# Kernel tuning notes

Measured on AMD Instinct MI355X. Metric: run time of the kernel, lower is better.

Reference implementation:

```python
import jax, jax.numpy as jnp
import numpy as np

B, L, FD = 16, 196, 2048      # batch, fmap locations (14x14), resnet101 feat dim
N, WD, HD, DD = 1000, 300, 512, 5  # n_class, word_dim, hid_dim, d_dim
E, TMAX, NIMG = 50000, 5, 1000     # n_edges, gru steps, imagenet classes


def setup_inputs():
    key = jax.random.key(0)
    ks = jax.random.split(key, 32)
    p = lambda k, s: (jax.random.normal(k, s, jnp.float32) * 0.02)
    z = lambda n: jnp.zeros((n,), jnp.float32)
    return {
        'feats': jax.random.normal(ks[0], (B, L, FD), jnp.float32),
        'embed': jax.random.normal(ks[1], (N, WD), jnp.float32),
        'edges': jax.random.randint(ks[2], (2, E), 0, N, jnp.int32),
        # attention key/query nets
        'W_key': p(ks[3], (FD, HD)), 'b_key': z(HD),
        'W_query': p(ks[4], (WD, HD)), 'b_query': z(HD),
        # F_in: feat_dim -> 512 -> d_dim (relu)
        'Wf1': p(ks[5], (FD, 512)), 'bf1': z(512),
        'Wf2': p(ks[6], (512, DD)), 'bf2': z(DD),
        # F_rel: 2*word_dim -> 256 -> 1 (relu)
        'Wr1': p(ks[7], (2 * WD, 256)), 'br1': z(256),
        'Wr2': p(ks[8], (256, 1)), 'br2': z(1),
        # F_out: d_dim -> 512 -> 1 (relu)
        'Wo1': p(ks[9], (DD, 512)), 'bo1': z(512),
        'Wo2': p(ks[10], (512, 1)), 'bo2': z(1),
        # GRUCell (torch layout: [3*d, d] stacked r,z,n)
        'W_ih': p(ks[11], (3 * DD, DD)), 'b_ih': z(3 * DD),
        'W_hh': p(ks[12], (3 * DD, DD)), 'b_hh': z(3 * DD),
        # imagenet classifier on pooled features
        'W_clf': p(ks[13], (FD, NIMG)), 'b_clf': z(NIMG),
    }


def _gru_cell(x, h, W_ih, W_hh, b_ih, b_hh):
    gi = x @ W_ih.T + b_ih            # [M, 3d]
    gh = h @ W_hh.T + b_hh
    i_r, i_z, i_n = jnp.split(gi, 3, axis=-1)
    h_r, h_z, h_n = jnp.split(gh, 3, axis=-1)
    r = jax.nn.sigmoid(i_r + h_r)
    zg = jax.nn.sigmoid(i_z + h_z)
    n = jnp.tanh(i_n + r * h_n)
    return (1.0 - zg) * n + zg * h


def reference(feats, embed, edges, W_key, b_key, W_query, b_query,
              Wf1, bf1, Wf2, bf2, Wr1, br1, Wr2, br2, Wo1, bo1, Wo2, bo2,
              W_ih, b_ih, W_hh, b_hh, W_clf, b_clf):
    # imagenet scores from globally pooled backbone features
    pooled = jnp.mean(feats, axis=1)                      # [B, FD]
    imgnet_scores = jax.nn.softmax(pooled @ W_clf + b_clf, axis=1)

    # label-conditional spatial attention
    keys = feats @ W_key + b_key                          # [B, L, HD]
    queries = embed @ W_query + b_query                   # [N, HD]
    scores = jnp.einsum('blh,nh->bnl', keys, queries)     # [B, N, L]
    attn = jax.nn.softmax(scores, axis=2)
    graph_input = jnp.einsum('bnl,blf->bnf', attn, feats) # [B, N, FD]
    graph_input = graph_input.reshape(-1, FD)             # [B*N, FD]

    # F_in MLP -> initial hidden state
    h0 = jax.nn.relu(graph_input @ Wf1 + bf1) @ Wf2 + bf2  # [B*N, DD]

    # edge weights from word-embedding pairs, scattered into dense [N, N]
    et = jnp.concatenate([embed[edges[0]], embed[edges[1]]], axis=1)  # [E, 2*WD]
    vals = jnp.tanh((jax.nn.relu(et @ Wr1 + br1) @ Wr2 + br2).reshape(-1))
    prop_mat = jnp.zeros((N, N), jnp.float32).at[edges[0], edges[1]].add(vals)

    # t_max message-passing + GRU steps (sequential recurrence)
    def step(hidden, _):
        msg = jnp.tanh(jnp.einsum('nm,bmd->bnd', prop_mat,
                                  hidden.reshape(B, N, DD))).reshape(-1, DD)
        return _gru_cell(msg, hidden, W_ih, W_hh, b_ih, b_hh), None
    hidden, _ = jax.lax.scan(step, h0, None, length=TMAX)

    logits = (jax.nn.relu(hidden @ Wo1 + bo1) @ Wo2 + bo2).reshape(B, N)
    return logits, attn, imgnet_scores
```

## Files before the change

kernel.cpp:

```cpp
#include <hip/hip_runtime.h>
#include <hip/hip_bf16.h>
#include <math.h>

#define B_   16
#define L_   196
#define FD_  2048
#define N_   1000
#define WD_  300
#define HD_  512
#define DD_  5
#define E_   50000
#define TMAX_ 5
#define NIMG_ 1000
#define WDP_ 320
#define LP_  224
#define EKP_ 640

typedef __attribute__((ext_vector_type(8))) short bf16x8;
typedef __attribute__((ext_vector_type(4))) float f32x4;

#define SMEM_MEGA1    49152
#define SMEM_MM_SPLIT 49152
#define SMEM_MM_NS    24576
#define SMEM_PREP     4352

#define SBAR()    asm volatile("s_barrier" ::: "memory")
#define WVM(N)    asm volatile("s_waitcnt vmcnt(" #N ")" ::: "memory")

__device__ __forceinline__ short bf_hi(float x) {
    unsigned u = __float_as_uint(x);
    unsigned r = u + 0x7fffu + ((u >> 16) & 1u);
    return (short)(r >> 16);
}
__device__ __forceinline__ float bf2f_(short s) {
    return __uint_as_float(((unsigned)(unsigned short)s) << 16);
}

__device__ __forceinline__ void gl16(const short* g, char* l) {
    __builtin_amdgcn_global_load_lds(
        (const __attribute__((address_space(1))) void*)g,
        (__attribute__((address_space(3))) void*)l, 16, 0, 0);
}

#define OUT_SPLIT 1
#define OUT_SC    2
#define OUT_F1T   3
#define OUT_H0    4

template<int OUTMODE, bool SPLIT>
__device__ __forceinline__ void mm_core(
    char* sm, int bx, int by, int zb,
    const short* __restrict__ Ah, const short* __restrict__ Al,
    const short* __restrict__ Bh, const short* __restrict__ Bl,
    const float* __restrict__ bias, void* __restrict__ C0, void* __restrict__ C1,
    void* __restrict__ C2, const float* __restrict__ W2,
    int M, int N, int K, int kbeg, int kend)
{
    const int PBUF = SPLIT ? 24576 : 12288;
    char* AsH = sm;
    char* AsL = sm + 8192;
    char* BsH = sm + (SPLIT ? 16384 : 8192);
    char* BsL = sm + 20480;
    int t = threadIdx.x;
    int lane = t & 63, w = t >> 6;
    int q = lane >> 4, r = lane & 15;
    int row0 = by * 128, col0 = bx * 64;

    int srow = t >> 2, cd = t & 3;
    int cg = cd ^ ((srow >> 1) & 3);
    int gA0 = row0 + srow;       if (gA0 >= M) gA0 = M - 1;
    int gA1 = row0 + 64 + srow;  if (gA1 >= M) gA1 = M - 1;
    int gB  = col0 + srow;       if (gB  >= N) gB  = N - 1;
    const short* pA0 = Ah + (long)gA0 * K + cg * 8 + kbeg;
    const short* pA1 = Ah + (long)gA1 * K + cg * 8 + kbeg;
    const short* pB  = Bh + (long)gB  * K + cg * 8 + kbeg;
    const short* pA0l = Ah; const short* pA1l = Ah; const short* pBl = Bh;
    if (SPLIT) {
        pA0l = Al + (long)gA0 * K + cg * 8 + kbeg;
        pA1l = Al + (long)gA1 * K + cg * 8 + kbeg;
        pBl  = Bl + (long)gB  * K + cg * 8 + kbeg;
    }
    char* dA0 = AsH + t * 16;
    char* dA1 = AsH + 4096 + t * 16;
    char* dB  = BsH + t * 16;
    char* dA0l = AsL + t * 16;
    char* dA1l = AsL + 4096 + t * 16;
    char* dBl  = BsL + t * 16;

    int x = (q ^ ((r >> 1) & 3)) * 16;
    int aoff0 = (w * 32 + r) * 64 + x;
    int aoff1 = aoff0 + 1024;
    int boff[4];
    #pragma unroll
    for (int ct = 0; ct < 4; ct++) boff[ct] = (ct * 16 + r) * 64 + x;

    f32x4 zero4 = {0.f, 0.f, 0.f, 0.f};
    f32x4 acc[2][4];
    #pragma unroll
    for (int i = 0; i < 2; i++)
        #pragma unroll
        for (int j = 0; j < 4; j++) acc[i][j] = zero4;

    auto stage = [&](int ks) {
        int off = (ks & 1) * PBUF;
        int ko = ks * 32;
        gl16(pA0 + ko, dA0 + off);
        gl16(pA1 + ko, dA1 + off);
        gl16(pB  + ko, dB  + off);
        if (SPLIT) {
            gl16(pA0l + ko, dA0l + off);
            gl16(pA1l + ko, dA1l + off);
            gl16(pBl  + ko, dBl  + off);
        }
    };

    int nk = (kend - kbeg) >> 5;
    stage(0);
    for (int ks = 0; ks < nk; ks++) {
        if (ks + 1 < nk) {
            stage(ks + 1);
            if (SPLIT) { WVM(6); } else { WVM(3); }
        } else {
            WVM(0);
        }
        SBAR();

        int cur = (ks & 1) * PBUF;
        bf16x8 ah0 = *(const bf16x8*)(AsH + cur + aoff0);
        bf16x8 ah1 = *(const bf16x8*)(AsH + cur + aoff1);
        bf16x8 al0, al1;
        if (SPLIT) {
            al0 = *(const bf16x8*)(AsL + cur + aoff0);
            al1 = *(const bf16x8*)(AsL + cur + aoff1);
        }
        #pragma unroll
        for (int ct = 0; ct < 4; ct++) {
            bf16x8 bh = *(const bf16x8*)(BsH + cur + boff[ct]);
            acc[0][ct] = __builtin_amdgcn_mfma_f32_16x16x32_bf16(ah0, bh, acc[0][ct], 0, 0, 0);
            acc[1][ct] = __builtin_amdgcn_mfma_f32_16x16x32_bf16(ah1, bh, acc[1][ct], 0, 0, 0);
            if (SPLIT) {
                acc[0][ct] = __builtin_amdgcn_mfma_f32_16x16x32_bf16(al0, bh, acc[0][ct], 0, 0, 0);
                acc[1][ct] = __builtin_amdgcn_mfma_f32_16x16x32_bf16(al1, bh, acc[1][ct], 0, 0, 0);
                bf16x8 bl = *(const bf16x8*)(BsL + cur + boff[ct]);
                acc[0][ct] = __builtin_amdgcn_mfma_f32_16x16x32_bf16(ah0, bl, acc[0][ct], 0, 0, 0);
                acc[1][ct] = __builtin_amdgcn_mfma_f32_16x16x32_bf16(ah1, bl, acc[1][ct], 0, 0, 0);
            }
        }
        if (ks + 1 < nk) SBAR();
    }

    if (OUTMODE == OUT_H0) {
        float s[2][4][DD_];
        #pragma unroll
        for (int i = 0; i < 2; i++)
            #pragma unroll
            for (int reg = 0; reg < 4; reg++)
                #pragma unroll
                for (int d = 0; d < DD_; d++) s[i][reg][d] = 0.f;
        #pragma unroll
        for (int i = 0; i < 2; i++) {
            #pragma unroll
            for (int ct = 0; ct < 4; ct++) {
                int n = col0 + ct * 16 + r;
                float w2v[DD_];
                #pragma unroll
                for (int d = 0; d < DD_; d++) w2v[d] = W2[n * DD_ + d];
                float b1 = bias[n];
                #pragma unroll
                for (int reg = 0; reg < 4; reg++) {
                    int m = row0 + w * 32 + i * 16 + q * 4 + reg;
                    if (m >= M) continue;
                    float val = fmaxf(acc[i][ct][reg] + b1, 0.f);
                    #pragma unroll
                    for (int d = 0; d < DD_; d++) s[i][reg][d] = fmaf(val, w2v[d], s[i][reg][d]);
                }
            }
        }
        #pragma unroll
        for (int i = 0; i < 2; i++)
            #pragma unroll
            for (int reg = 0; reg < 4; reg++)
                #pragma unroll
                for (int d = 0; d < DD_; d++) {
                    float v = s[i][reg][d];
                    v += __shfl_xor(v, 1);
                    v += __shfl_xor(v, 2);
                    v += __shfl_xor(v, 4);
                    v += __shfl_xor(v, 8);
                    if (r == 0) {
                        int m = row0 + w * 32 + i * 16 + q * 4 + reg;
                        if (m < M)
                            atomicAdd(&((float*)C0)[(long)m * (B_ * DD_) + zb * DD_ + d], v);
                    }
                }
        return;
    }

    #pragma unroll
    for (int i = 0; i < 2; i++) {
        #pragma unroll
        for (int ct = 0; ct < 4; ct++) {
            #pragma unroll
            for (int reg = 0; reg < 4; reg++) {
                int m = row0 + w * 32 + i * 16 + q * 4 + reg;
                int n = col0 + ct * 16 + r;
                if (m >= M || n >= N) continue;
                float v = acc[i][ct][reg];
                if (OUTMODE == OUT_SC) {
                    ((float*)C0)[(long)m * N + n] = v;
                } else if (OUTMODE == OUT_F1T) {
                    int b = m / 196, l = m - b * 196;
                    ((short*)C2)[((long)b * 512 + n) * LP_ + l] = bf_hi(v);
                } else {
                    float v2 = v + bias[n];
                    long idx = (long)m * N + n;
                    short hi = bf_hi(v2);
                    ((short*)C0)[idx] = hi;
                    ((short*)C1)[idx] = bf_hi(v2 - bf2f_(hi));
                }
            }
        }
    }
}

__device__ __forceinline__ void edge_core(
    char* sm, int be,
    const short* __restrict__ embedH, const int* __restrict__ edges,
    const short* __restrict__ Wr1T, const float* __restrict__ br1,
    const float* __restrict__ Wr2, const float* __restrict__ br2,
    float* __restrict__ prop)
{
    const int EPBUF = 20480;
    char* As = sm;
    char* Bs = sm + 4096;
    int* src = (int*)(sm + 40960);
    int* dst = (int*)(sm + 41216);
    float (*part)[5] = (float(*)[5])(sm + 41472);
    int t = threadIdx.x;
    int e0 = be * 64;
    if (t < 64) {
        int e = e0 + t;
        src[t] = (e < E_) ? edges[e] : 0;
        dst[t] = (e < E_) ? edges[E_ + e] : 0;
    }
    __syncthreads();
    int lane = t & 63, w = t >> 6, q = lane >> 4, r = lane & 15;
    f32x4 zero4 = {0.f, 0.f, 0.f, 0.f};
    f32x4 acc[4][4];
    #pragma unroll
    for (int i = 0; i < 4; i++)
        #pragma unroll
        for (int j = 0; j < 4; j++) acc[i][j] = zero4;

    int srow = t >> 2, cd = t & 3;
    int cg = cd ^ ((srow >> 1) & 3);
    const short* baseS = embedH + (long)src[srow] * WDP_ + cg * 8;
    const short* baseD = embedH + (long)dst[srow] * WDP_ + cg * 8;
    const short* pB = Wr1T + (long)srow * EKP_ + cg * 8;
    char* dA = As + t * 16;
    char* dB = Bs + t * 16;

    int x = (q ^ ((r >> 1) & 3)) * 16;
    int aoff[4], boff[4];
    #pragma unroll
    for (int i = 0; i < 4; i++) {
        aoff[i] = (i * 16 + r) * 64 + x;
        boff[i] = (w * 64 + i * 16 + r) * 64 + x;
    }

    auto estage = [&](int ks) {
        int off = (ks & 1) * EPBUF;
        const short* pa = (ks < 10) ? baseS + ks * 32 : baseD + (ks - 10) * 32;
        gl16(pa, dA + off);
        #pragma unroll
        for (int i = 0; i < 4; i++)
            gl16(pB + (long)i * 64 * EKP_ + ks * 32, dB + i * 4096 + off);
    };

    estage(0);
    for (int ks = 0; ks < 20; ks++) {
        if (ks + 1 < 20) {
            estage(ks + 1);
            WVM(5);
        } else {
            WVM(0);
        }
        SBAR();

        int cur = (ks & 1) * EPBUF;
        bf16x8 af[4], bfr[4];
        #pragma unroll
        for (int rt = 0; rt < 4; rt++) af[rt] = *(const bf16x8*)(As + cur + aoff[rt]);
        #pragma unroll
        for (int ct = 0; ct < 4; ct++) bfr[ct] = *(const bf16x8*)(Bs + cur + boff[ct]);
        #pragma unroll
        for (int rt = 0; rt < 4; rt++)
            #pragma unroll
            for (int ct = 0; ct < 4; ct++)
                acc[rt][ct] = __builtin_amdgcn_mfma_f32_16x16x32_bf16(af[rt], bfr[ct], acc[rt][ct], 0, 0, 0);
        if (ks + 1 < 20) SBAR();
    }
    float b1v[4], w2v[4];
    #pragma unroll
    for (int ct = 0; ct < 4; ct++) {
        int u = w * 64 + ct * 16 + r;
        b1v[ct] = br1[u];
        w2v[ct] = Wr2[u];
    }
    #pragma unroll
    for (int rt = 0; rt < 4; rt++) {
        #pragma unroll
        for (int reg = 0; reg < 4; reg++) {
            float s = 0.f;
            #pragma unroll
            for (int ct = 0; ct < 4; ct++)
                s = fmaf(fmaxf(acc[rt][ct][reg] + b1v[ct], 0.f), w2v[ct], s);
            s += __shfl_xor(s, 1);
            s += __shfl_xor(s, 2);
            s += __shfl_xor(s, 4);
            s += __shfl_xor(s, 8);
            if (r == 0) part[rt * 16 + q * 4 + reg][w] = s;
        }
    }
    __syncthreads();
    if (t < 64 && e0 + t < E_) {
        float s = part[t][0] + part[t][1] + part[t][2] + part[t][3];
        atomicAdd(&prop[(long)src[t] * N_ + dst[t]], tanhf(s + br2[0]));
    }
}

__device__ __forceinline__ void transconv_core(
    char* sm, int bx, int by,
    const float* __restrict__ in, short* __restrict__ outH, short* __restrict__ outL,
    int Kd, int N, int Ks)
{
    float (*tile)[33] = (float(*)[33])sm;
    int k0 = bx * 32, n0 = by * 32;
    int t = threadIdx.x;
    int tr = t >> 5, tc = t & 31;
    #pragma unroll
    for (int i = 0; i < 4; i++) {
        int k = k0 + tr + i * 8, n = n0 + tc;
        tile[tr + i * 8][tc] = (k < Kd && n < N) ? in[(long)k * N + n] : 0.f;
    }
    __syncthreads();
    #pragma unroll
    for (int i = 0; i < 4; i++) {
        int n = n0 + tr + i * 8, k = k0 + tc;
        if (n < N && k < Ks) {
            float x = tile[tc][tr + i * 8];
            short hi = bf_hi(x);
            outH[(long)n * Ks + k] = hi;
            if (outL) outL[(long)n * Ks + k] = bf_hi(x - bf2f_(hi));
        }
    }
}

__global__ __launch_bounds__(256) void prep(
    float* __restrict__ prop, float* __restrict__ Ht0, const float* __restrict__ bf2,
    const float* __restrict__ feats, float* __restrict__ pooled,
    short* __restrict__ featsH, short* __restrict__ featsL,
    const float* __restrict__ embed, short* __restrict__ embH, short* __restrict__ embL,
    const float* __restrict__ W_key, const float* __restrict__ Wf1,
    short* __restrict__ WkfH, short* __restrict__ WkfL,
    const float* __restrict__ W_query, short* __restrict__ WqTh, short* __restrict__ WqTl,
    const float* __restrict__ Wr1, short* __restrict__ Wr1T, short* __restrict__ F1T)
{
    __shared__ __align__(16) char sm[SMEM_PREP];
    int b = blockIdx.x, t = threadIdx.x;
    if (b < 977) {
        int i = (b * 256 + t) * 4;
        if (i < N_ * N_) { float4 z = {0.f, 0.f, 0.f, 0.f}; *(float4*)(prop + i) = z; }
    } else if (b < 1290) {
        int i = (b - 977) * 256 + t;
        if (i < N_ * B_ * DD_) Ht0[i] = bf2[i % DD_];
    } else if (b < 1418) {
        int idx = (b - 1290) * 256 + t;
        int bb = idx / FD_, f = idx % FD_;
        const float* p = feats + (long)bb * L_ * FD_ + f;
        float acc = 0.f;
        for (int l = 0; l < L_; l++) acc += p[(long)l * FD_];
        pooled[idx] = acc * (1.0f / L_);
    } else if (b < 4554) {
        long i = ((long)(b - 1418) * 256 + t) * 8;
        float4 v0 = *(const float4*)(feats + i);
        float4 v1 = *(const float4*)(feats + i + 4);
        float xs[8] = {v0.x, v0.y, v0.z, v0.w, v1.x, v1.y, v1.z, v1.w};
        short h[8], l8[8];
        #pragma unroll
        for (int j = 0; j < 8; j++) {
            h[j] = bf_hi(xs[j]);
            l8[j] = bf_hi(xs[j] - bf2f_(h[j]));
        }
        *(int4*)(featsH + i) = *(int4*)h;
        *(int4*)(featsL + i) = *(int4*)l8;
    } else if (b < 4867) {
        int i = ((b - 4554) * 256 + t) * 4;
        if (i < N_ * WDP_) {
            int n = i / WDP_, c = i - n * WDP_;
            short h[4], l4[4];
            if (c < WD_) {
                float4 v = *(const float4*)(embed + (long)n * WD_ + c);
                float xs[4] = {v.x, v.y, v.z, v.w};
                #pragma unroll
                for (int j = 0; j < 4; j++) {
                    h[j] = bf_hi(xs[j]);
                    l4[j] = bf_hi(xs[j] - bf2f_(h[j]));
                }
            } else {
                #pragma unroll
                for (int j = 0; j < 4; j++) { h[j] = 0; l4[j] = 0; }
            }
            *(int2*)(embH + (long)n * WDP_ + c) = *(int2*)h;
            *(int2*)(embL + (long)n * WDP_ + c) = *(int2*)l4;
        }
    } else if (b < 5891) {
        int bb = b - 4867;
        transconv_core(sm, bb % 64, bb / 64, W_key, WkfH, WkfL, FD_, HD_, FD_);
    } else if (b < 6915) {
        int bb = b - 5891;
        transconv_core(sm, bb % 64, bb / 64, Wf1, WkfH + (size_t)512 * FD_, nullptr, FD_, HD_, FD_);
    } else if (b < 7075) {
        int bb = b - 6915;
        transconv_core(sm, bb % 10, bb / 10, W_query, WqTh, WqTl, WD_, HD_, WDP_);
    } else if (b < 7235) {
        int bb = b - 7075;
        int bx = bb % 20, by = bb / 20;
        float (*tile)[33] = (float(*)[33])sm;
        int k0 = bx * 32, n0 = by * 32;
        int tr = t >> 5, tc = t & 31;
        #pragma unroll
        for (int i = 0; i < 4; i++) {
            int kout = k0 + tr + i * 8, n = n0 + tc;
            int kin = (kout < 320) ? kout : kout - 20;
            bool valid = (kout < 320) ? (kout < 300) : (kout < 620);
            tile[tr + i * 8][tc] = valid ? Wr1[(long)kin * 256 + n] : 0.f;
        }
        __syncthreads();
        #pragma unroll
        for (int i = 0; i < 4; i++) {
            int n = n0 + tr + i * 8, k = k0 + tc;
            Wr1T[(long)n * EKP_ + k] = bf_hi(tile[tc][tr + i * 8]);
        }
    } else {
        int idx = (b - 7235) * 256 + t;
        int row = idx / 7, j = idx - row * 7;
        int2 z2; z2.x = 0; z2.y = 0;
        *(int2*)(F1T + (long)row * LP_ + 196 + j * 4) = z2;
    }
}

__global__ __launch_bounds__(256) void mega1(
    const short* __restrict__ featsH, const short* __restrict__ featsL,
    const short* __restrict__ WkfH, const short* __restrict__ WkfL,
    const float* __restrict__ b_key, short* __restrict__ keysH, short* __restrict__ keysL,
    short* __restrict__ F1T,
    const short* __restrict__ embH, const short* __restrict__ embL,
    const short* __restrict__ WqTh, const short* __restrict__ WqTl,
    const float* __restrict__ b_query, short* __restrict__ qH, short* __restrict__ qL,
    const int* __restrict__ edges, const short* __restrict__ Wr1T,
    const float* __restrict__ br1, const float* __restrict__ Wr2,
    const float* __restrict__ br2, float* __restrict__ prop,
    const float* __restrict__ pooled, const float* __restrict__ W_clf,
    const float* __restrict__ b_clf, float* __restrict__ Pimg)
{
    __shared__ __align__(16) char sm[SMEM_MEGA1];
    int b = blockIdx.x;
    if (b < 200) {
        int l = (b & 7) * 25 + (b >> 3);
        mm_core<OUT_SPLIT, true>(sm, l & 7, l >> 3, 0,
            featsH, featsL, WkfH, WkfL, b_key,
            keysH, keysL, nullptr, nullptr, B_ * L_, 512, FD_, 0, FD_);
    } else if (b < 400) {
        int bb = b - 200;
        int l = (bb & 7) * 25 + (bb >> 3);
        mm_core<OUT_F1T, false>(sm, l & 7, l >> 3, 0,
            featsH, nullptr, WkfH + (size_t)512 * FD_, nullptr, nullptr,
            nullptr, nullptr, F1T, nullptr, B_ * L_, 512, FD_, 0, FD_);
    } else if (b < 464) {
        int bb = b - 400;
        int l = (bb & 7) * 8 + (bb >> 3);
        mm_core<OUT_SPLIT, true>(sm, l & 7, l >> 3, 0,
            embH, embL, WqTh, WqTl, b_query,
            qH, qL, nullptr, nullptr, N_, HD_, WDP_, 0, WDP_);
    } else if (b < 1246) {
        edge_core(sm, b - 464, embH, edges, Wr1T, br1, Wr2, br2, prop);
    } else {
        int bb = b - 1246;
        int ks = bb / 63, ix = bb % 63;
        int i = ix * 256 + threadIdx.x;
        if (i < B_ * NIMG_) {
            int bi = i / NIMG_, n = i % NIMG_;
            const float* p = pooled + (long)bi * FD_ + ks * 256;
            const float* w = W_clf + (long)(ks * 256) * NIMG_ + n;
            float acc = (ks == 0) ? b_clf[n] : 0.f;
            #pragma unroll 4
            for (int k = 0; k < 256; k++) acc = fmaf(p[k], w[(long)k * NIMG_], acc);
            Pimg[(long)ks * (B_ * NIMG_) + i] = acc;
        }
    }
}

__global__ __launch_bounds__(256) void mega2(
    const short* __restrict__ qH, const short* __restrict__ qL,
    const short* __restrict__ keysH, const short* __restrict__ keysL,
    float* __restrict__ Pattn,
    const float* __restrict__ Pimg, float* __restrict__ out_img)
{
    __shared__ __align__(16) char sm[SMEM_MM_SPLIT];
    int b = blockIdx.x;
    if (b < 512) {
        int l = (b & 7) * 64 + (b >> 3);
        int zb = l >> 5, by = (l >> 2) & 7, bx = l & 3;
        const short* Bh = keysH + (long)zb * L_ * HD_;
        const short* Bl = keysL + (long)zb * L_ * HD_;
        float* C0 = Pattn + (long)zb * N_ * L_;
        mm_core<OUT_SC, true>(sm, bx, by, 0, qH, qL, Bh, Bl, nullptr,
                              C0, nullptr, nullptr, nullptr,
                              N_, L_, HD_, 0, HD_);
    } else {
        int t = threadIdx.x;
        int wave = (b - 512) * 4 + (t >> 6), lane = t & 63;
        if (wave >= B_) return;
        const int PER = (NIMG_ + 63) / 64;
        float v[PER];
        float m = -1e30f;
        int cnt = 0;
        for (int k = lane; k < NIMG_; k += 64) {
            float s = 0.f;
            #pragma unroll
            for (int ks = 0; ks < 8; ks++) s += Pimg[(long)ks * (B_ * NIMG_) + wave * NIMG_ + k];
            v[cnt] = s; m = fmaxf(m, s); cnt++;
        }
        #pragma unroll
        for (int off = 32; off; off >>= 1) m = fmaxf(m, __shfl_xor(m, off));
        float s = 0.f;
        for (int i = 0; i < cnt; i++) { v[i] = expf(v[i] - m); s += v[i]; }
        #pragma unroll
        for (int off = 32; off; off >>= 1) s += __shfl_xor(s, off);
        float inv = 1.f / s;
        cnt = 0;
        for (int k = lane; k < NIMG_; k += 64) out_img[(long)wave * NIMG_ + k] = v[cnt++] * inv;
    }
}

__global__ void softmax_attn(const float* __restrict__ P0,
                             float* __restrict__ X, short* __restrict__ Xb, int rows)
{
    int gid = blockIdx.x * blockDim.x + threadIdx.x;
    int wave = gid >> 6, lane = gid & 63;
    if (wave >= rows) return;
    const int PER = (L_ + 63) / 64;
    float v[PER];
    float m = -1e30f;
    int cnt = 0;
    for (int k = lane; k < L_; k += 64) {
        v[cnt] = P0[(long)wave * L_ + k];
        m = fmaxf(m, v[cnt]); cnt++;
    }
    #pragma unroll
    for (int off = 32; off; off >>= 1) m = fmaxf(m, __shfl_xor(m, off));
    float s = 0.f;
    for (int i = 0; i < cnt; i++) { v[i] = expf(v[i] - m); s += v[i]; }
    #pragma unroll
    for (int off = 32; off; off >>= 1) s += __shfl_xor(s, off);
    float inv = 1.f / s;
    cnt = 0;
    for (int k = lane; k < L_; k += 64) {
        float val = v[cnt++] * inv;
        X[(long)wave * L_ + k] = val;
        Xb[(long)wave * LP_ + k] = bf_hi(val);
    }
    if (lane < LP_ - L_) Xb[(long)wave * LP_ + L_ + lane] = 0;
}

__global__ __launch_bounds__(256) void h0gemm(
    const short* __restrict__ attnH, const short* __restrict__ F1T,
    const float* __restrict__ bf1, const float* __restrict__ Wf2,
    float* __restrict__ Ht0)
{
    __shared__ __align__(16) char sm[SMEM_MM_NS];
    int b = blockIdx.x;
    int l = (b & 7) * 128 + (b >> 3);
    int zb = l >> 6, by = (l >> 3) & 7, bx = l & 7;
    const short* Ap = attnH + (long)zb * N_ * LP_;
    const short* Bp = F1T + (long)zb * HD_ * LP_;
    mm_core<OUT_H0, false>(sm, bx, by, zb, Ap, nullptr, Bp, nullptr,
                           bf1, Ht0, nullptr, nullptr, Wf2,
                           N_, HD_, LP_, 0, LP_);
}

__global__ __launch_bounds__(640) void step_kernel(
    const float* __restrict__ prop, const float* __restrict__ Hin,
    float* __restrict__ Hout,
    const float* __restrict__ W_ih, const float* __restrict__ b_ih,
    const float* __restrict__ W_hh, const float* __restrict__ b_hh)
{
    __shared__ float msg[2][4][80];
    int t = threadIdx.x;
    int half = t / 320, tt = t - half * 320;
    int nl = tt / 80, c = tt - nl * 80;
    int n = blockIdx.x * 4 + nl;
    const float* pr = prop + (long)n * N_ + half * 500;
    const float* hc = Hin + c + (long)half * 500 * 80;
    float a0 = 0.f, a1 = 0.f, a2 = 0.f, a3 = 0.f;
    #pragma unroll 4
    for (int m4 = 0; m4 < 500; m4 += 4) {
        float4 pv = *(const float4*)(pr + m4);
        a0 = fmaf(pv.x, hc[(long)(m4 + 0) * 80], a0);
        a1 = fmaf(pv.y, hc[(long)(m4 + 1) * 80], a1);
        a2 = fmaf(pv.z, hc[(long)(m4 + 2) * 80], a2);
        a3 = fmaf(pv.w, hc[(long)(m4 + 3) * 80], a3);
    }
    msg[half][nl][c] = (a0 + a1) + (a2 + a3);
    __syncthreads();
    if (t < 320) {
        int nl2 = t / 80, c2 = t - nl2 * 80;
        msg[0][nl2][c2] = tanhf(msg[0][nl2][c2] + msg[1][nl2][c2]);
    }
    __syncthreads();
    if (t < 64) {
        int nl2 = t >> 4, b = t & 15;
        int n2 = blockIdx.x * 4 + nl2;
        float xv[DD_], h[DD_];
        #pragma unroll
        for (int j = 0; j < DD_; j++) {
            xv[j] = msg[0][nl2][b * DD_ + j];
            h[j] = Hin[(long)n2 * 80 + b * DD_ + j];
        }
        float gi[3 * DD_], gh[3 * DD_];
        #pragma unroll
        for (int g = 0; g < 3 * DD_; g++) {
            float a = b_ih[g], cc = b_hh[g];
            #pragma unroll
            for (int k = 0; k < DD_; k++) {
                a = fmaf(xv[k], W_ih[g * DD_ + k], a);
                cc = fmaf(h[k], W_hh[g * DD_ + k], cc);
            }
            gi[g] = a; gh[g] = cc;
        }
        #pragma unroll
        for (int j = 0; j < DD_; j++) {
            float rr = 1.f / (1.f + expf(-(gi[j] + gh[j])));
            float zz = 1.f / (1.f + expf(-(gi[DD_ + j] + gh[DD_ + j])));
            float nn2 = tanhf(gi[2 * DD_ + j] + rr * gh[2 * DD_ + j]);
            Hout[(long)n2 * 80 + b * DD_ + j] = (1.f - zz) * nn2 + zz * h[j];
        }
    }
}

__global__ void out_kernel(const float* __restrict__ ht, const float* __restrict__ Wo1,
                           const float* __restrict__ bo1, const float* __restrict__ Wo2,
                           const float* __restrict__ bo2, float* __restrict__ logits, int rows)
{
    int gid = blockIdx.x * blockDim.x + threadIdx.x;
    int wave = gid >> 6, lane = gid & 63;
    if (wave >= rows) return;
    int b = wave / N_, n = wave % N_;
    float x[DD_];
    #pragma unroll
    for (int i = 0; i < DD_; i++) x[i] = ht[(long)n * (B_ * DD_) + b * DD_ + i];
    float acc = 0.f;
    for (int j = lane; j < HD_; j += 64) {
        float h = bo1[j];
        #pragma unroll
        for (int d = 0; d < DD_; d++) h = fmaf(x[d], Wo1[d * HD_ + j], h);
        h = fmaxf(h, 0.f);
        acc = fmaf(h, Wo2[j], acc);
    }
    #pragma unroll
    for (int off = 32; off; off >>= 1) acc += __shfl_down(acc, off);
    if (lane == 0) logits[wave] = acc + bo2[0];
}

extern "C" void kernel_launch(void* const* d_in, const int* in_sizes, int n_in,
                              void* d_out, int out_size, void* d_ws, size_t ws_size,
                              hipStream_t stream)
{
    const float* feats   = (const float*)d_in[0];
    const float* embed   = (const float*)d_in[1];
    const int*   edges   = (const int*)  d_in[2];
    const float* W_key   = (const float*)d_in[3];
    const float* b_key   = (const float*)d_in[4];
    const float* W_query = (const float*)d_in[5];
    const float* b_query = (const float*)d_in[6];
    const float* Wf1     = (const float*)d_in[7];
    const float* bf1     = (const float*)d_in[8];
    const float* Wf2     = (const float*)d_in[9];
    const float* bf2     = (const float*)d_in[10];
    const float* Wr1     = (const float*)d_in[11];
    const float* br1     = (const float*)d_in[12];
    const float* Wr2     = (const float*)d_in[13];
    const float* br2     = (const float*)d_in[14];
    const float* Wo1     = (const float*)d_in[15];
    const float* bo1     = (const float*)d_in[16];
    const float* Wo2     = (const float*)d_in[17];
    const float* bo2     = (const float*)d_in[18];
    const float* W_ih    = (const float*)d_in[19];
    const float* b_ih    = (const float*)d_in[20];
    const float* W_hh    = (const float*)d_in[21];
    const float* b_hh    = (const float*)d_in[22];
    const float* W_clf   = (const float*)d_in[23];
    const float* b_clf   = (const float*)d_in[24];

    float* out_logits = (float*)d_out;
    float* out_attn   = out_logits + B_ * N_;
    float* out_img    = out_attn + (long)B_ * N_ * L_;

    char* p = (char*)d_ws;
    auto alloc = [&](size_t bytes) { void* r = (void*)p; p += (bytes + 255) & ~(size_t)255; return r; };
    float* pooled  = (float*)alloc((size_t)B_ * FD_ * 4);
    short* featsH  = (short*)alloc((size_t)B_ * L_ * FD_ * 2);
    short* featsL  = (short*)alloc((size_t)B_ * L_ * FD_ * 2);
    short* WkfH    = (short*)alloc((size_t)1024 * FD_ * 2);
    short* WkfL    = (short*)alloc((size_t)512 * FD_ * 2);
    short* WqTh    = (short*)alloc((size_t)HD_ * WDP_ * 2);
    short* WqTl    = (short*)alloc((size_t)HD_ * WDP_ * 2);
    short* Wr1T    = (short*)alloc((size_t)256 * EKP_ * 2);
    short* embH    = (short*)alloc((size_t)N_ * WDP_ * 2);
    short* embL    = (short*)alloc((size_t)N_ * WDP_ * 2);
    short* keysH   = (short*)alloc((size_t)B_ * L_ * HD_ * 2);
    short* keysL   = (short*)alloc((size_t)B_ * L_ * HD_ * 2);
    short* qH      = (short*)alloc((size_t)N_ * HD_ * 2);
    short* qL      = (short*)alloc((size_t)N_ * HD_ * 2);
    short* attnH   = (short*)alloc((size_t)B_ * N_ * LP_ * 2);
    short* F1T     = (short*)alloc((size_t)B_ * HD_ * LP_ * 2);
    float* prop    = (float*)alloc((size_t)N_ * N_ * 4);
    float* Ht0     = (float*)alloc((size_t)N_ * B_ * DD_ * 4);
    float* Ht1     = (float*)alloc((size_t)N_ * B_ * DD_ * 4);
    float* Pimg    = (float*)alloc((size_t)8 * B_ * NIMG_ * 4);
    float* Pattn   = (float*)alloc((size_t)B_ * N_ * L_ * 4);

    prep<<<7459, 256, 0, stream>>>(prop, Ht0, bf2, feats, pooled, featsH, featsL,
                                   embed, embH, embL, W_key, Wf1, WkfH, WkfL,
                                   W_query, WqTh, WqTl, Wr1, Wr1T, F1T);

    mega1<<<1750, 256, 0, stream>>>(featsH, featsL, WkfH, WkfL, b_key, keysH, keysL, F1T,
                                    embH, embL, WqTh, WqTl, b_query, qH, qL,
                                    edges, Wr1T, br1, Wr2, br2, prop,
                                    pooled, W_clf, b_clf, Pimg);

    mega2<<<516, 256, 0, stream>>>(qH, qL, keysH, keysL, Pattn, Pimg, out_img);

    softmax_attn<<<(B_ * N_ * 64 + 255) / 256, 256, 0, stream>>>(
        Pattn, out_attn, attnH, B_ * N_);

    h0gemm<<<1024, 256, 0, stream>>>(attnH, F1T, bf1, Wf2, Ht0);

    {
        float* hin = Ht0;
        float* hout = Ht1;
        for (int step = 0; step < TMAX_; step++) {
            step_kernel<<<N_ / 4, 640, 0, stream>>>(prop, hin, hout,
                                                    W_ih, b_ih, W_hh, b_hh);
            float* tmp = hin; hin = hout; hout = tmp;
        }
        out_kernel<<<(B_ * N_ * 64 + 255) / 256, 256, 0, stream>>>(hin, Wo1, bo1, Wo2, bo2,
                                                                   out_logits, B_ * N_);
    }
}
```

Before: 439.4 us.

## Vectorize pooling, tile classifier, LDS-stage step kernel, batch output MLP rows

The mean-pooling prep blocks now read float4 and each thread covers four features, which cuts that block range from 128 to 32 blocks. The ImageNet classifier partial now stages pooled rows in LDS and computes all 16 batch rows per thread, so each W_clf load is reused 16 times and mega1 needs fewer blocks. step_kernel drops the two-half 640-thread split and instead stages chunks of Hin and prop in LDS at 320 threads, with extra barriers per chunk. out_kernel caches Wo1, bo1 and Wo2 in LDS and handles 16 rows per wave instead of one.

```diff
diff --git a/kernel.cpp b/kernel.cpp
--- a/kernel.cpp
+++ b/kernel.cpp
@@ -374,15 +374,20 @@
     } else if (b < 1290) {
         int i = (b - 977) * 256 + t;
         if (i < N_ * B_ * DD_) Ht0[i] = bf2[i % DD_];
-    } else if (b < 1418) {
+    } else if (b < 1322) {
         int idx = (b - 1290) * 256 + t;
-        int bb = idx / FD_, f = idx % FD_;
-        const float* p = feats + (long)bb * L_ * FD_ + f;
-        float acc = 0.f;
-        for (int l = 0; l < L_; l++) acc += p[(long)l * FD_];
-        pooled[idx] = acc * (1.0f / L_);
-    } else if (b < 4554) {
-        long i = ((long)(b - 1418) * 256 + t) * 8;
+        int bb = idx >> 9, f4 = (idx & 511) * 4;
+        const float* p = feats + (long)bb * L_ * FD_ + f4;
+        float4 acc = {0.f, 0.f, 0.f, 0.f};
+        for (int l = 0; l < L_; l++) {
+            float4 v = *(const float4*)(p + (long)l * FD_);
+            acc.x += v.x; acc.y += v.y; acc.z += v.z; acc.w += v.w;
+        }
+        const float inv = 1.0f / L_;
+        acc.x *= inv; acc.y *= inv; acc.z *= inv; acc.w *= inv;
+        *(float4*)(pooled + (long)bb * FD_ + f4) = acc;
+    } else if (b < 4458) {
+        long i = ((long)(b - 1322) * 256 + t) * 8;
         float4 v0 = *(const float4*)(feats + i);
         float4 v1 = *(const float4*)(feats + i + 4);
         float xs[8] = {v0.x, v0.y, v0.z, v0.w, v1.x, v1.y, v1.z, v1.w};
@@ -394,8 +399,8 @@
         }
         *(int4*)(featsH + i) = *(int4*)h;
         *(int4*)(featsL + i) = *(int4*)l8;
-    } else if (b < 4867) {
-        int i = ((b - 4554) * 256 + t) * 4;
+    } else if (b < 4771) {
+        int i = ((b - 4458) * 256 + t) * 4;
         if (i < N_ * WDP_) {
             int n = i / WDP_, c = i - n * WDP_;
             short h[4], l4[4];
@@ -414,17 +419,17 @@
             *(int2*)(embH + (long)n * WDP_ + c) = *(int2*)h;
             *(int2*)(embL + (long)n * WDP_ + c) = *(int2*)l4;
         }
-    } else if (b < 5891) {
-        int bb = b - 4867;
+    } else if (b < 5795) {
+        int bb = b - 4771;
         transconv_core(sm, bb % 64, bb / 64, W_key, WkfH, WkfL, FD_, HD_, FD_);
-    } else if (b < 6915) {
-        int bb = b - 5891;
+    } else if (b < 6819) {
+        int bb = b - 5795;
         transconv_core(sm, bb % 64, bb / 64, Wf1, WkfH + (size_t)512 * FD_, nullptr, FD_, HD_, FD_);
-    } else if (b < 7075) {
-        int bb = b - 6915;
+    } else if (b < 6979) {
+        int bb = b - 6819;
         transconv_core(sm, bb % 10, bb / 10, W_query, WqTh, WqTl, WD_, HD_, WDP_);
-    } else if (b < 7235) {
-        int bb = b - 7075;
+    } else if (b < 7139) {
+        int bb = b - 6979;
         int bx = bb % 20, by = bb / 20;
         float (*tile)[33] = (float(*)[33])sm;
         int k0 = bx * 32, n0 = by * 32;
@@ -443,7 +448,7 @@
             Wr1T[(long)n * EKP_ + k] = bf_hi(tile[tc][tr + i * 8]);
         }
     } else {
-        int idx = (b - 7235) * 256 + t;
+        int idx = (b - 7139) * 256 + t;
         int row = idx / 7, j = idx - row * 7;
         int2 z2; z2.x = 0; z2.y = 0;
         *(int2*)(F1T + (long)row * LP_ + 196 + j * 4) = z2;
@@ -487,16 +492,31 @@
         edge_core(sm, b - 464, embH, edges, Wr1T, br1, Wr2, br2, prop);
     } else {
         int bb = b - 1246;
-        int ks = bb / 63, ix = bb % 63;
-        int i = ix * 256 + threadIdx.x;
-        if (i < B_ * NIMG_) {
-            int bi = i / NIMG_, n = i % NIMG_;
-            const float* p = pooled + (long)bi * FD_ + ks * 256;
-            const float* w = W_clf + (long)(ks * 256) * NIMG_ + n;
-            float acc = (ks == 0) ? b_clf[n] : 0.f;
+        int ks = bb >> 2, nb = bb & 3;
+        float* poolLds = (float*)sm;
+        int t = threadIdx.x;
+        for (int id = t; id < 1024; id += 256) {
+            int bi = id >> 6, koff = (id & 63) * 4;
+            *(float4*)&poolLds[bi * 256 + koff] =
+                *(const float4*)(pooled + (long)bi * FD_ + ks * 256 + koff);
+        }
+        __syncthreads();
+        int n = nb * 256 + t;
+        if (n < NIMG_) {
+            float acc[16];
+            #pragma unroll
+            for (int bi = 0; bi < 16; bi++) acc[bi] = 0.f;
             #pragma unroll 4
-            for (int k = 0; k < 256; k++) acc = fmaf(p[k], w[(long)k * NIMG_], acc);
-            Pimg[(long)ks * (B_ * NIMG_) + i] = acc;
+            for (int k = 0; k < 256; k++) {
+                float wv = W_clf[(long)(ks * 256 + k) * NIMG_ + n];
+                #pragma unroll
+                for (int bi = 0; bi < 16; bi++)
+                    acc[bi] = fmaf(poolLds[bi * 256 + k], wv, acc[bi]);
+            }
+            float bc = (ks == 0) ? b_clf[n] : 0.f;
+            #pragma unroll
+            for (int bi = 0; bi < 16; bi++)
+                Pimg[(long)ks * (B_ * NIMG_) + bi * NIMG_ + n] = acc[bi] + bc;
         }
     }
 }
@@ -590,34 +610,40 @@
                            N_, HD_, LP_, 0, LP_);
 }
 
-__global__ __launch_bounds__(640) void step_kernel(
+__global__ __launch_bounds__(320) void step_kernel(
     const float* __restrict__ prop, const float* __restrict__ Hin,
     float* __restrict__ Hout,
     const float* __restrict__ W_ih, const float* __restrict__ b_ih,
     const float* __restrict__ W_hh, const float* __restrict__ b_hh)
 {
-    __shared__ float msg[2][4][80];
+    __shared__ float hinLds[100][80];
+    __shared__ float propLds[4][100];
+    __shared__ float msg[4][80];
     int t = threadIdx.x;
-    int half = t / 320, tt = t - half * 320;
-    int nl = tt / 80, c = tt - nl * 80;
-    int n = blockIdx.x * 4 + nl;
-    const float* pr = prop + (long)n * N_ + half * 500;
-    const float* hc = Hin + c + (long)half * 500 * 80;
+    int nl = t / 80, c = t - nl * 80;
     float a0 = 0.f, a1 = 0.f, a2 = 0.f, a3 = 0.f;
-    #pragma unroll 4
-    for (int m4 = 0; m4 < 500; m4 += 4) {
-        float4 pv = *(const float4*)(pr + m4);
-        a0 = fmaf(pv.x, hc[(long)(m4 + 0) * 80], a0);
-        a1 = fmaf(pv.y, hc[(long)(m4 + 1) * 80], a1);
-        a2 = fmaf(pv.z, hc[(long)(m4 + 2) * 80], a2);
-        a3 = fmaf(pv.w, hc[(long)(m4 + 3) * 80], a3);
-    }
-    msg[half][nl][c] = (a0 + a1) + (a2 + a3);
-    __syncthreads();
-    if (t < 320) {
-        int nl2 = t / 80, c2 = t - nl2 * 80;
-        msg[0][nl2][c2] = tanhf(msg[0][nl2][c2] + msg[1][nl2][c2]);
-    }
+    for (int ch = 0; ch < 10; ch++) {
+        int m0 = ch * 100;
+        for (int id = t; id < 2000; id += 320) {
+            int m = id / 20, coff = (id % 20) * 4;
+            *(float4*)&hinLds[m][coff] = *(const float4*)(Hin + (long)(m0 + m) * 80 + coff);
+        }
+        if (t < 100) {
+            int pn = t / 25, poff = (t % 25) * 4;
+            *(float4*)&propLds[pn][poff] =
+                *(const float4*)(prop + (long)(blockIdx.x * 4 + pn) * N_ + m0 + poff);
+        }
+        __syncthreads();
+        #pragma unroll 5
+        for (int m4 = 0; m4 < 100; m4 += 4) {
+            a0 = fmaf(propLds[nl][m4 + 0], hinLds[m4 + 0][c], a0);
+            a1 = fmaf(propLds[nl][m4 + 1], hinLds[m4 + 1][c], a1);
+            a2 = fmaf(propLds[nl][m4 + 2], hinLds[m4 + 2][c], a2);
+            a3 = fmaf(propLds[nl][m4 + 3], hinLds[m4 + 3][c], a3);
+        }
+        __syncthreads();
+    }
+    msg[nl][c] = tanhf((a0 + a1) + (a2 + a3));
     __syncthreads();
     if (t < 64) {
         int nl2 = t >> 4, b = t & 15;
@@ -625,7 +651,7 @@
         float xv[DD_], h[DD_];
         #pragma unroll
         for (int j = 0; j < DD_; j++) {
-            xv[j] = msg[0][nl2][b * DD_ + j];
+            xv[j] = msg[nl2][b * DD_ + j];
             h[j] = Hin[(long)n2 * 80 + b * DD_ + j];
         }
         float gi[3 * DD_], gh[3 * DD_];
@@ -649,28 +675,44 @@
     }
 }
 
-__global__ void out_kernel(const float* __restrict__ ht, const float* __restrict__ Wo1,
-                           const float* __restrict__ bo1, const float* __restrict__ Wo2,
-                           const float* __restrict__ bo2, float* __restrict__ logits, int rows)
-{
-    int gid = blockIdx.x * blockDim.x + threadIdx.x;
-    int wave = gid >> 6, lane = gid & 63;
-    if (wave >= rows) return;
-    int b = wave / N_, n = wave % N_;
-    float x[DD_];
-    #pragma unroll
-    for (int i = 0; i < DD_; i++) x[i] = ht[(long)n * (B_ * DD_) + b * DD_ + i];
-    float acc = 0.f;
-    for (int j = lane; j < HD_; j += 64) {
-        float h = bo1[j];
-        #pragma unroll
-        for (int d = 0; d < DD_; d++) h = fmaf(x[d], Wo1[d * HD_ + j], h);
-        h = fmaxf(h, 0.f);
-        acc = fmaf(h, Wo2[j], acc);
-    }
-    #pragma unroll
-    for (int off = 32; off; off >>= 1) acc += __shfl_down(acc, off);
-    if (lane == 0) logits[wave] = acc + bo2[0];
+__global__ __launch_bounds__(256) void out_kernel(
+    const float* __restrict__ ht, const float* __restrict__ Wo1,
+    const float* __restrict__ bo1, const float* __restrict__ Wo2,
+    const float* __restrict__ bo2, float* __restrict__ logits, int rows)
+{
+    __shared__ float w1[DD_][HD_];
+    __shared__ float w2[HD_];
+    __shared__ float b1[HD_];
+    int t = threadIdx.x;
+    for (int j = t; j < HD_; j += 256) {
+        w2[j] = Wo2[j];
+        b1[j] = bo1[j];
+        #pragma unroll
+        for (int d = 0; d < DD_; d++) w1[d][j] = Wo1[d * HD_ + j];
+    }
+    __syncthreads();
+    int wv = t >> 6, lane = t & 63;
+    float bo2v = bo2[0];
+    #pragma unroll
+    for (int rr = 0; rr < 16; rr++) {
+        int row = blockIdx.x * 64 + wv * 16 + rr;
+        if (row >= rows) break;
+        int b = row / N_, n = row - b * N_;
+        float x[DD_];
+        #pragma unroll
+        for (int i = 0; i < DD_; i++) x[i] = ht[(long)n * (B_ * DD_) + b * DD_ + i];
+        float acc = 0.f;
+        for (int j = lane; j < HD_; j += 64) {
+            float h = b1[j];
+            #pragma unroll
+            for (int d = 0; d < DD_; d++) h = fmaf(x[d], w1[d][j], h);
+            h = fmaxf(h, 0.f);
+            acc = fmaf(h, w2[j], acc);
+        }
+        #pragma unroll
+        for (int off = 32; off; off >>= 1) acc += __shfl_down(acc, off);
+        if (lane == 0) logits[row] = acc + bo2v;
+    }
 }
 
 extern "C" void kernel_launch(void* const* d_in, const int* in_sizes, int n_in,
@@ -731,11 +773,11 @@
     float* Pimg    = (float*)alloc((size_t)8 * B_ * NIMG_ * 4);
     float* Pattn   = (float*)alloc((size_t)B_ * N_ * L_ * 4);
 
-    prep<<<7459, 256, 0, stream>>>(prop, Ht0, bf2, feats, pooled, featsH, featsL,
+    prep<<<7363, 256, 0, stream>>>(prop, Ht0, bf2, feats, pooled, featsH, featsL,
                                    embed, embH, embL, W_key, Wf1, WkfH, WkfL,
                                    W_query, WqTh, WqTl, Wr1, Wr1T, F1T);
 
-    mega1<<<1750, 256, 0, stream>>>(featsH, featsL, WkfH, WkfL, b_key, keysH, keysL, F1T,
+    mega1<<<1278, 256, 0, stream>>>(featsH, featsL, WkfH, WkfL, b_key, keysH, keysL, F1T,
                                     embH, embL, WqTh, WqTl, b_query, qH, qL,
                                     edges, Wr1T, br1, Wr2, br2, prop,
                                     pooled, W_clf, b_clf, Pimg);
@@ -751,11 +793,11 @@
         float* hin = Ht0;
         float* hout = Ht1;
         for (int step = 0; step < TMAX_; step++) {
-            step_kernel<<<N_ / 4, 640, 0, stream>>>(prop, hin, hout,
+            step_kernel<<<N_ / 4, 320, 0, stream>>>(prop, hin, hout,
                                                     W_ih, b_ih, W_hh, b_hh);
             float* tmp = hin; hin = hout; hout = tmp;
         }
-        out_kernel<<<(B_ * N_ * 64 + 255) / 256, 256, 0, stream>>>(hin, Wo1, bo1, Wo2, bo2,
-                                                                   out_logits, B_ * N_);
-    }
-}
+        out_kernel<<<250, 256, 0, stream>>>(hin, Wo1, bo1, Wo2, bo2,
+                                            out_logits, B_ * N_);
+    }
+}
```

Result: slower. 517.9 us (+17.9%).
